# Performance work log

Measured on AMD Instinct MI355X. Metric: run time of the kernel, lower is better.

## Reference

```python
import jax, jax.numpy as jnp
import numpy as np

# model dims (see init_kwargs)
HID = 2048
H = 16
Q_LORA = 768
KV_LORA = 512
QK_NOPE = 128
QK_ROPE = 64
QK_HEAD = QK_NOPE + QK_ROPE  # 192
V_DIM = 128
HI = 8        # indexer heads
DI = 128      # indexer head dim
TOPK = 512    # index_topk
EPS = 1e-5
B, S = 1, 2048


def rms_norm(x, w):
    return x * jax.lax.rsqrt(jnp.mean(x * x, -1, keepdims=True) + EPS) * w


def layer_norm(x, w, b):
    m = jnp.mean(x, -1, keepdims=True)
    v = jnp.mean((x - m) ** 2, -1, keepdims=True)
    return (x - m) * jax.lax.rsqrt(v + EPS) * w + b


def rotate_half(x):
    x1, x2 = jnp.split(x, 2, axis=-1)
    return jnp.concatenate([-x2, x1], axis=-1)


def rope_bshd(x, cos, sin):
    # x: [B,S,H,D], cos/sin: [B,S,D] -> broadcast over heads (unsqueeze_dim=2)
    return x * cos[:, :, None, :] + rotate_half(x) * sin[:, :, None, :]


def setup_inputs() -> dict:
    key = jax.random.key(0)
    ks = jax.random.split(key, 16)
    std = 0.02
    hidden_states = jax.random.normal(ks[0], (B, S, HID), jnp.float32)
    # real RoPE tables, theta=10000, head_dim=QK_ROPE
    inv_freq = 1.0 / (10000.0 ** (np.arange(0, QK_ROPE, 2, dtype=np.float32) / QK_ROPE))
    freqs = np.arange(S, dtype=np.float32)[:, None] * inv_freq[None, :]  # [S, ROPE/2]
    emb = np.concatenate([freqs, freqs], axis=-1)
    cos = jnp.asarray(np.cos(emb))[None]  # [1,S,ROPE]
    sin = jnp.asarray(np.sin(emb))[None]
    w = lambda k, shp: jax.random.normal(k, shp, jnp.float32) * std
    return {
        'hidden_states': hidden_states, 'cos': cos, 'sin': sin,
        'wq_a': w(ks[1], (Q_LORA, HID)),
        'q_a_norm_w': jnp.ones((Q_LORA,), jnp.float32),
        'wq_b': w(ks[2], (H * QK_HEAD, Q_LORA)),
        'wkv_a': w(ks[3], (KV_LORA + QK_ROPE, HID)),
        'kv_a_norm_w': jnp.ones((KV_LORA,), jnp.float32),
        'wkv_b': w(ks[4], (H * (QK_NOPE + V_DIM), KV_LORA)),
        'wo': w(ks[5], (HID, H * V_DIM)),
        'idx_wq_b': w(ks[6], (HI * DI, Q_LORA)),
        'idx_wk': w(ks[7], (DI, HID)),
        'idx_k_norm_w': jnp.ones((DI,), jnp.float32),
        'idx_k_norm_b': jnp.zeros((DI,), jnp.float32),
        'idx_weights_w': w(ks[8], (HI, HID)),
    }


def reference(hidden_states, cos, sin, wq_a, q_a_norm_w, wq_b, wkv_a, kv_a_norm_w,
              wkv_b, wo, idx_wq_b, idx_wk, idx_k_norm_w, idx_k_norm_b, idx_weights_w):
    b, s, _ = hidden_states.shape
    # ---- MLA projections ----
    q_lora = rms_norm(hidden_states @ wq_a.T, q_a_norm_w)              # [B,S,Q_LORA]
    q = (q_lora @ wq_b.T).reshape(b, s, H, QK_HEAD)
    q_nope, q_rope = jnp.split(q, [QK_NOPE], axis=-1)
    q_rope = rope_bshd(q_rope, cos, sin)

    kv = hidden_states @ wkv_a.T                                        # [B,S,KV_LORA+ROPE]
    kv_lat, k_rope = jnp.split(kv, [KV_LORA], axis=-1)
    k_rope = k_rope * cos + rotate_half(k_rope) * sin                   # shared MQA rope key [B,S,ROPE]
    kv_lat = rms_norm(kv_lat, kv_a_norm_w)
    kvb = (kv_lat @ wkv_b.T).reshape(b, s, H, QK_NOPE + V_DIM)
    k_nope, value = jnp.split(kvb, [QK_NOPE], axis=-1)

    queries = jnp.concatenate([q_nope, q_rope], axis=-1)                # [B,S,H,QK_HEAD]
    keys = jnp.concatenate(
        [k_nope, jnp.broadcast_to(k_rope[:, :, None, :], (b, s, H, QK_ROPE))], axis=-1)

    # ---- lightning indexer (DSA): per-query top-k KV selection ----
    iq = (q_lora @ idx_wq_b.T).reshape(b, s, HI, DI)
    iq_rot, iq_pass = jnp.split(iq, [QK_ROPE], axis=-1)
    iq = jnp.concatenate([rope_bshd(iq_rot, cos, sin), iq_pass], axis=-1)
    ik = layer_norm(hidden_states @ idx_wk.T, idx_k_norm_w, idx_k_norm_b)  # [B,S,DI]
    ik_rot, ik_pass = jnp.split(ik, [QK_ROPE], axis=-1)
    ik = jnp.concatenate([ik_rot * cos + rotate_half(ik_rot) * sin, ik_pass], axis=-1)

    iscores = jnp.einsum('bqhd,bkd->bqhk', iq, ik) * (DI ** -0.5)       # [B,S,HI,S]
    iw = (hidden_states @ idx_weights_w.T) * (HI ** -0.5)               # [B,S,HI]
    iscore = jnp.einsum('bqh,bqhk->bqk', iw, iscores)                   # [B,S,S]

    causal = jnp.tril(jnp.ones((s, s), bool))
    iscore = jnp.where(causal[None], iscore, -1e9)
    _, topk_idx = jax.lax.top_k(iscore, TOPK)                           # [B,S,TOPK]
    allow = jnp.zeros((b, s, s), bool).at[
        jnp.arange(b)[:, None, None], jnp.arange(s)[None, :, None], topk_idx].set(True)
    allow = allow & causal[None]                                        # topk AND causal

    # ---- masked attention ----
    scale = QK_HEAD ** -0.5
    scores = jnp.einsum('bqhd,bkhd->bhqk', queries, keys) * scale       # [B,H,S,S]
    scores = jnp.where(allow[:, None], scores, -jnp.inf)
    probs = jax.nn.softmax(scores, axis=-1)
    out = jnp.einsum('bhqk,bkhd->bqhd', probs, value).reshape(b, s, H * V_DIM)
    return out @ wo.T
```

## Files before the change

kernel.cpp:

```cpp
#include <hip/hip_runtime.h>
#include <hip/hip_bf16.h>
#include <stdint.h>
#include <math.h>

#define S_LEN 2048
#define HIDDEN 2048
#define NHEAD 16
#define QLORA 768
#define KVLORA 512
#define QKNOPE 128
#define QKROPE 64
#define QKHEAD 192
#define VDIM 128
#define HIN 8
#define DIN 128
#define TOPKN 512
#define EPSF 1e-5f
#define DLAT 576
#define SCALE_ATT 0.07216878364870322f

typedef __bf16 bf16x8 __attribute__((ext_vector_type(8)));
typedef float  f32x4  __attribute__((ext_vector_type(4)));

static __device__ __forceinline__ float wave_reduce_sum(float v) {
    #pragma unroll
    for (int off = 32; off > 0; off >>= 1) v += __shfl_down(v, off);
    return v;
}

static __device__ __forceinline__ void splitw(__bf16* __restrict__ H,
                                              __bf16* __restrict__ L,
                                              size_t idx, float v) {
    __bf16 h = (__bf16)v;
    H[idx] = h;
    L[idx] = (__bf16)(v - (float)h);
}

#define PREP_BLOCKS 17280
__global__ __launch_bounds__(256) void prep_all(
        const float* __restrict__ hid,     __bf16* hidH,  __bf16* hidL,
        const float* __restrict__ wq_a,    __bf16* wqaH,  __bf16* wqaL,
        const float* __restrict__ idx_wq_b,__bf16* iwqH,  __bf16* iwqL,
        const float* __restrict__ idx_wk,  __bf16* iwkH,  __bf16* iwkL,
        const float* __restrict__ wq_b,    __bf16* wq_b_bf,
        const float* __restrict__ wkv_a,   __bf16* wkv_a_bf,
        const float* __restrict__ wkv_b,   __bf16* wkv_b_bf,
        const float* __restrict__ wo,      __bf16* wo_bf,
        __bf16* wknt) {
    int b = blockIdx.x, tid = threadIdx.x;
    const float* src; __bf16 *dH = nullptr, *dL = nullptr, *dC = nullptr;
    int base;
    if (b < 4096)        { src = hid;      dH = hidH; dL = hidL; base = b; }
    else if (b < 5632)   { src = wq_a;     dH = wqaH; dL = wqaL; base = b - 4096; }
    else if (b < 6400)   { src = idx_wq_b; dH = iwqH; dL = iwqL; base = b - 5632; }
    else if (b < 6656)   { src = idx_wk;   dH = iwkH; dL = iwkL; base = b - 6400; }
    else if (b < 8960)   { src = wq_b;     dC = wq_b_bf;  base = b - 6656; }
    else if (b < 10112)  { src = wkv_a;    dC = wkv_a_bf; base = b - 8960; }
    else if (b < 12160)  { src = wkv_b;    dC = wkv_b_bf; base = b - 10112; }
    else if (b < 16256)  { src = wo;       dC = wo_bf;    base = b - 12160; }
    else {
        int e = ((b - 16256) * 256 + tid) * 4;
        int c = e & 511, d = (e >> 9) & 127, h = e >> 16;
        f32x4 v = *(const f32x4*)(wkv_b + ((size_t)(h * 256 + d)) * 512 + c);
        #pragma unroll
        for (int j = 0; j < 4; ++j)
            wknt[(size_t)h * 65536 + (c + j) * 128 + d] = (__bf16)v[j];
        return;
    }
    int i = (base * 256 + tid) * 4;
    f32x4 v = *(const f32x4*)(src + i);
    if (dC) {
        #pragma unroll
        for (int j = 0; j < 4; ++j) dC[i + j] = (__bf16)v[j];
    } else {
        #pragma unroll
        for (int j = 0; j < 4; ++j) splitw(dH, dL, i + j, v[j]);
    }
}

#define GBM 128
#define GBN 64
#define GBK 32
template <typename OutT>
static __device__ __forceinline__ void gemm_s_core(
        const __bf16* __restrict__ A, const __bf16* __restrict__ B,
        OutT* __restrict__ C, int K, int lda, int ldb, int ldc,
        int bx, int by) {
    __shared__ __bf16 sAs[GBM * GBK];
    __shared__ __bf16 sBs[GBN * GBK];
    int tid = threadIdx.x;
    int lane = tid & 63, wid = tid >> 6;
    int quad = lane >> 4, l16 = lane & 15;
    int wm = wid >> 1, wn = wid & 1;
    int row0 = by * GBM, col0 = bx * GBN;

    f32x4 acc[4][2] = {};
    int am = tid >> 1, ah = tid & 1;
    int bn = tid >> 2, bq = tid & 3;

    for (int k0 = 0; k0 < K; k0 += GBK) {
        const uint4* ga = (const uint4*)(A + (size_t)(row0 + am) * lda + k0 + ah * 16);
        uint4* da = (uint4*)&sAs[am * GBK + ah * 16];
        da[0] = ga[0];
        da[1] = ga[1];
        *(uint4*)&sBs[bn * GBK + bq * 8] =
            *(const uint4*)(B + (size_t)(col0 + bn) * ldb + k0 + bq * 8);
        __syncthreads();
        bf16x8 af[4], bfr[2];
        #pragma unroll
        for (int mi = 0; mi < 4; ++mi)
            af[mi] = *(const bf16x8*)&sAs[(wm * 64 + mi * 16 + l16) * GBK + quad * 8];
        #pragma unroll
        for (int ni = 0; ni < 2; ++ni)
            bfr[ni] = *(const bf16x8*)&sBs[(wn * 32 + ni * 16 + l16) * GBK + quad * 8];
        #pragma unroll
        for (int mi = 0; mi < 4; ++mi)
            #pragma unroll
            for (int ni = 0; ni < 2; ++ni)
                acc[mi][ni] = __builtin_amdgcn_mfma_f32_16x16x32_bf16(
                    af[mi], bfr[ni], acc[mi][ni], 0, 0, 0);
        __syncthreads();
    }
    #pragma unroll
    for (int mi = 0; mi < 4; ++mi)
        #pragma unroll
        for (int ni = 0; ni < 2; ++ni)
            #pragma unroll
            for (int r = 0; r < 4; ++r) {
                int row = row0 + wm * 64 + mi * 16 + quad * 4 + r;
                int col = col0 + wn * 32 + ni * 16 + l16;
                C[(size_t)row * ldc + col] = (OutT)acc[mi][ni][r];
            }
}

template <typename OutT>
__global__ __launch_bounds__(256) void gemm_s(const __bf16* __restrict__ A,
                                              const __bf16* __restrict__ B,
                                              OutT* __restrict__ C,
                                              int K, int lda, int ldb, int ldc,
                                              long sA, long sB, long sC) {
    gemm_s_core<OutT>(A + (size_t)blockIdx.z * sA, B + (size_t)blockIdx.z * sB,
                      C + (size_t)blockIdx.z * sC, K, lda, ldb, ldc,
                      blockIdx.x, blockIdx.y);
}

template <bool CAUSAL>
static __device__ __forceinline__ void gemm3_core(
        const __bf16* __restrict__ Ah, const __bf16* __restrict__ Al,
        const __bf16* __restrict__ Bh, const __bf16* __restrict__ Bl,
        float* __restrict__ C, int K, int lda, int ldb, int ldc,
        int row_base, int bx, int by) {
    int row0 = by * GBM + row_base, col0 = bx * GBN;
    if (CAUSAL && col0 > row0 + GBM - 1) return;
    __shared__ __bf16 sAh[GBM * GBK], sAl[GBM * GBK];
    __shared__ __bf16 sBh[GBN * GBK], sBl[GBN * GBK];
    int tid = threadIdx.x;
    int lane = tid & 63, wid = tid >> 6;
    int quad = lane >> 4, l16 = lane & 15;
    int wm = wid >> 1, wn = wid & 1;

    f32x4 acc[4][2] = {};
    int am = tid >> 1, ah = tid & 1;
    int bn = tid >> 2, bq = tid & 3;

    for (int k0 = 0; k0 < K; k0 += GBK) {
        size_t aoff = (size_t)(row0 + am) * lda + k0 + ah * 16;
        uint4* dah = (uint4*)&sAh[am * GBK + ah * 16];
        uint4* dal = (uint4*)&sAl[am * GBK + ah * 16];
        dah[0] = ((const uint4*)(Ah + aoff))[0];
        dah[1] = ((const uint4*)(Ah + aoff))[1];
        dal[0] = ((const uint4*)(Al + aoff))[0];
        dal[1] = ((const uint4*)(Al + aoff))[1];
        size_t boff = (size_t)(col0 + bn) * ldb + k0 + bq * 8;
        *(uint4*)&sBh[bn * GBK + bq * 8] = *(const uint4*)(Bh + boff);
        *(uint4*)&sBl[bn * GBK + bq * 8] = *(const uint4*)(Bl + boff);
        __syncthreads();
        bf16x8 afh[4], afl[4], bfh[2], bfl[2];
        #pragma unroll
        for (int mi = 0; mi < 4; ++mi) {
            int o = (wm * 64 + mi * 16 + l16) * GBK + quad * 8;
            afh[mi] = *(const bf16x8*)&sAh[o];
            afl[mi] = *(const bf16x8*)&sAl[o];
        }
        #pragma unroll
        for (int ni = 0; ni < 2; ++ni) {
            int o = (wn * 32 + ni * 16 + l16) * GBK + quad * 8;
            bfh[ni] = *(const bf16x8*)&sBh[o];
            bfl[ni] = *(const bf16x8*)&sBl[o];
        }
        #pragma unroll
        for (int mi = 0; mi < 4; ++mi)
            #pragma unroll
            for (int ni = 0; ni < 2; ++ni) {
                acc[mi][ni] = __builtin_amdgcn_mfma_f32_16x16x32_bf16(
                    afl[mi], bfh[ni], acc[mi][ni], 0, 0, 0);
                acc[mi][ni] = __builtin_amdgcn_mfma_f32_16x16x32_bf16(
                    afh[mi], bfl[ni], acc[mi][ni], 0, 0, 0);
                acc[mi][ni] = __builtin_amdgcn_mfma_f32_16x16x32_bf16(
                    afh[mi], bfh[ni], acc[mi][ni], 0, 0, 0);
            }
        __syncthreads();
    }
    #pragma unroll
    for (int mi = 0; mi < 4; ++mi)
        #pragma unroll
        for (int ni = 0; ni < 2; ++ni)
            #pragma unroll
            for (int r = 0; r < 4; ++r) {
                int row = row0 + wm * 64 + mi * 16 + quad * 4 + r;
                int col = col0 + wn * 32 + ni * 16 + l16;
                C[(size_t)row * ldc + col] = acc[mi][ni][r];
            }
}

__global__ __launch_bounds__(256) void gemm3_ks(const __bf16* __restrict__ Ah,
                                                const __bf16* __restrict__ Al,
                                                const __bf16* __restrict__ Bh,
                                                const __bf16* __restrict__ Bl,
                                                float* __restrict__ Cpart,
                                                int Ksub, int lda, int ldb, int ldc,
                                                long sC) {
    int bz = blockIdx.z, koff = bz * Ksub;
    gemm3_core<false>(Ah + koff, Al + koff, Bh + koff, Bl + koff,
                      Cpart + (size_t)bz * sC, Ksub, lda, ldb, ldc, 0,
                      blockIdx.x, blockIdx.y);
}

__global__ __launch_bounds__(256) void fused_mid(
        const __bf16* __restrict__ qlH, const __bf16* __restrict__ qlL,
        const __bf16* __restrict__ wq_b_bf, __bf16* __restrict__ qbuf_bf,
        const __bf16* __restrict__ hidH, const __bf16* __restrict__ hidL,
        const __bf16* __restrict__ wkv_a_bf, float* __restrict__ kv,
        const __bf16* __restrict__ iwqH, const __bf16* __restrict__ iwqL,
        float* __restrict__ iqraw,
        const __bf16* __restrict__ iwkH, const __bf16* __restrict__ iwkL,
        float* __restrict__ ikraw) {
    int b = blockIdx.x;
    if (b < 768) {
        gemm_s_core<__bf16>(qlH, wq_b_bf, qbuf_bf, QLORA, QLORA, QLORA,
                            NHEAD * QKHEAD, b % 48, b / 48);
    } else if (b < 912) {
        int r = b - 768;
        gemm_s_core<float>(hidH, wkv_a_bf, kv, HIDDEN, HIDDEN, HIDDEN, DLAT,
                           r % 9, r / 9);
    } else if (b < 1168) {
        int r = b - 912;
        gemm3_core<false>(qlH, qlL, iwqH, iwqL, iqraw, QLORA, QLORA, QLORA,
                          HIN * DIN, 0, r & 15, r >> 4);
    } else {
        int r = b - 1168;
        gemm3_core<false>(hidH, hidL, iwkH, iwkL, ikraw, HIDDEN, HIDDEN, HIDDEN,
                          DIN, 0, r & 1, r >> 1);
    }
}

__global__ __launch_bounds__(256) void fused2(
        const __bf16* __restrict__ qbuf_bf, const __bf16* __restrict__ wknt,
        __bf16* __restrict__ qeff,
        const __bf16* __restrict__ cqH, const __bf16* __restrict__ cqL,
        const __bf16* __restrict__ ikH, const __bf16* __restrict__ ikL,
        float* __restrict__ iscore) {
    int b = blockIdx.x;
    if (b < 2048) {
        int bx = b & 7, by = (b >> 3) & 15, bz = b >> 7;
        gemm_s_core<__bf16>(qbuf_bf + bz * QKHEAD, wknt + (size_t)bz * 512 * 128,
                            qeff + bz * DLAT, 128, NHEAD * QKHEAD, 128,
                            NHEAD * DLAT, bx, by);
    } else {
        int r = b - 2048;
        gemm3_core<true>(cqH, cqL, ikH, ikL, iscore, DIN, DIN, DIN, S_LEN,
                         TOPKN, r & 31, r >> 5);
    }
}

__global__ __launch_bounds__(256) void rmsnorm_split4(const float* __restrict__ p,
                                                      long ps,
                                                      const float* __restrict__ w,
                                                      __bf16* __restrict__ yH,
                                                      __bf16* __restrict__ yL, int ncols) {
    int row = blockIdx.x, tid = threadIdx.x;
    const float* p0 = p + (size_t)row * ncols;
    float ss = 0.f;
    for (int c = tid; c < ncols; c += 256) {
        float v = p0[c] + p0[ps + c] + p0[2 * ps + c] + p0[3 * ps + c];
        ss += v * v;
    }
    __shared__ float red[4];
    ss = wave_reduce_sum(ss);
    if ((tid & 63) == 0) red[tid >> 6] = ss;
    __syncthreads();
    float tot = red[0] + red[1] + red[2] + red[3];
    float inv = rsqrtf(tot / (float)ncols + EPSF);
    for (int c = tid; c < ncols; c += 256) {
        float v = p0[c] + p0[ps + c] + p0[2 * ps + c] + p0[3 * ps + c];
        splitw(yH, yL, (size_t)row * ncols + c, v * inv * w[c]);
    }
}

__global__ __launch_bounds__(256) void fused_post(
        const __bf16* __restrict__ qbuf, __bf16* __restrict__ qeff,
        const float* __restrict__ kv, const float* __restrict__ kvw,
        __bf16* __restrict__ klat,
        const float* __restrict__ ikraw, const float* __restrict__ lnw,
        const float* __restrict__ lnb, __bf16* __restrict__ ikH, __bf16* __restrict__ ikL,
        const float* __restrict__ iqraw, const float* __restrict__ hid,
        const float* __restrict__ iww, __bf16* __restrict__ cqH, __bf16* __restrict__ cqL,
        const float* __restrict__ cosT, const float* __restrict__ sinT) {
    int s = blockIdx.x, tid = threadIdx.x;
    int lane = tid & 63, wid = tid >> 6;

    for (int i = tid; i < NHEAD * 32; i += 256) {
        int h = i >> 5, d = i & 31;
        const __bf16* base = qbuf + (size_t)s * (NHEAD * QKHEAD) + h * QKHEAD + QKNOPE;
        float x1 = (float)base[d], x2 = (float)base[d + 32];
        float c1 = cosT[s * 64 + d],      s1 = sinT[s * 64 + d];
        float c2 = cosT[s * 64 + d + 32], s2 = sinT[s * 64 + d + 32];
        __bf16* o = qeff + (size_t)s * (NHEAD * DLAT) + h * DLAT + 512;
        o[d]      = (__bf16)(x1 * c1 - x2 * s1);
        o[d + 32] = (__bf16)(x2 * c2 + x1 * s2);
    }

    {
        const float* row = kv + (size_t)s * DLAT;
        float ss = 0.f;
        for (int c = tid; c < KVLORA; c += 256) { float v = row[c]; ss += v * v; }
        __shared__ float redB[4];
        ss = wave_reduce_sum(ss);
        if (lane == 0) redB[wid] = ss;
        __syncthreads();
        float tot = redB[0] + redB[1] + redB[2] + redB[3];
        float inv = rsqrtf(tot / (float)KVLORA + EPSF);
        __bf16* orow = klat + (size_t)s * DLAT;
        for (int c = tid; c < KVLORA; c += 256)
            orow[c] = (__bf16)(row[c] * inv * kvw[c]);
        if (tid < 32) {
            int d = tid;
            float x1 = row[KVLORA + d], x2 = row[KVLORA + d + 32];
            float c1 = cosT[s * 64 + d],      s1 = sinT[s * 64 + d];
            float c2 = cosT[s * 64 + d + 32], s2 = sinT[s * 64 + d + 32];
            orow[512 + d]      = (__bf16)(x1 * c1 - x2 * s1);
            orow[512 + d + 32] = (__bf16)(x2 * c2 + x1 * s2);
        }
    }

    {
        float x = (tid < DIN) ? ikraw[(size_t)s * DIN + tid] : 0.f;
        __shared__ float redC1[4], redC2[4], sy[DIN];
        float sm = wave_reduce_sum(x);
        if (lane == 0) redC1[wid] = sm;
        __syncthreads();
        float mean = (redC1[0] + redC1[1] + redC1[2] + redC1[3]) / (float)DIN;
        float dx = (tid < DIN) ? (x - mean) : 0.f;
        float vs = wave_reduce_sum(dx * dx);
        if (lane == 0) redC2[wid] = vs;
        __syncthreads();
        float var = (redC2[0] + redC2[1] + redC2[2] + redC2[3]) / (float)DIN;
        if (tid < DIN) sy[tid] = dx * rsqrtf(var + EPSF) * lnw[tid] + lnb[tid];
        __syncthreads();
        size_t ro = (size_t)s * DIN;
        if (tid < 32) {
            int d = tid;
            float c1 = cosT[s * 64 + d],      s1 = sinT[s * 64 + d];
            float c2 = cosT[s * 64 + d + 32], s2 = sinT[s * 64 + d + 32];
            splitw(ikH, ikL, ro + d,      sy[d] * c1 - sy[d + 32] * s1);
            splitw(ikH, ikL, ro + d + 32, sy[d + 32] * c2 + sy[d] * s2);
        } else if (tid >= 64 && tid < DIN) {
            splitw(ikH, ikL, ro + tid, sy[tid]);
        }
        __syncthreads();
    }

    {
        __shared__ float redD[4][HIN], siw[HIN];
        float a8[HIN] = {};
        const float* xr = hid + (size_t)s * HIDDEN;
        for (int c = tid; c < HIDDEN; c += 256) {
            float x = xr[c];
            #pragma unroll
            for (int h = 0; h < HIN; ++h) a8[h] += x * iww[h * HIDDEN + c];
        }
        #pragma unroll
        for (int h = 0; h < HIN; ++h) a8[h] = wave_reduce_sum(a8[h]);
        if (lane == 0)
            #pragma unroll
            for (int h = 0; h < HIN; ++h) redD[wid][h] = a8[h];
        __syncthreads();
        if (tid < HIN)
            siw[tid] = redD[0][tid] + redD[1][tid] + redD[2][tid] + redD[3][tid];
        __syncthreads();
        if (tid < DIN) {
            int d = tid;
            float acc = 0.f;
            float c1 = 0.f, s1 = 0.f;
            if (d < 64) { c1 = cosT[s * 64 + d]; s1 = sinT[s * 64 + d]; }
            #pragma unroll
            for (int h = 0; h < HIN; ++h) {
                const float* base = iqraw + ((size_t)s * HIN + h) * DIN;
                float v;
                if (d < 32)       v = base[d] * c1 - base[d + 32] * s1;
                else if (d < 64)  v = base[d] * c1 + base[d - 32] * s1;
                else              v = base[d];
                acc += siw[h] * v;
            }
            splitw(cqH, cqL, (size_t)s * DIN + d, acc * 0.03125f);
        }
    }
}

__global__ __launch_bounds__(256) void topk_rows(const float* __restrict__ iscore,
                                                 int* __restrict__ topk) {
    int q = TOPKN + blockIdx.x;
    int n = q + 1;
    __shared__ uint32_t skey[S_LEN];
    __shared__ int hist[256];
    __shared__ int scan[256];
    __shared__ uint32_t sp;
    __shared__ int sr, pos;
    int tid = threadIdx.x;
    const float* row = iscore + (size_t)q * S_LEN;
    for (int i = tid; i < n; i += 256) {
        uint32_t u = __float_as_uint(row[i]);
        skey[i] = (u & 0x80000000u) ? ~u : (u | 0x80000000u);
    }
    __syncthreads();
    uint32_t prefix = 0;
    int remk = TOPKN;
    for (int pass = 0; pass < 4; ++pass) {
        int shift = 24 - 8 * pass;
        uint32_t pmask = pass ? (0xFFFFFFFFu << (shift + 8)) : 0u;
        hist[tid] = 0;
        __syncthreads();
        for (int i = tid; i < n; i += 256) {
            uint32_t u = skey[i];
            if ((u & pmask) == prefix) atomicAdd(&hist[(u >> shift) & 255], 1);
        }
        __syncthreads();
        scan[tid] = hist[tid];
        __syncthreads();
        for (int step = 1; step < 256; step <<= 1) {
            int v = (tid + step < 256) ? scan[tid + step] : 0;
            __syncthreads();
            scan[tid] += v;
            __syncthreads();
        }
        int Sb = scan[tid];
        int Snext = (tid < 255) ? scan[tid + 1] : 0;
        if (Sb >= remk && Snext < remk) {
            sp = prefix | ((uint32_t)tid << shift);
            sr = remk - Snext;
        }
        __syncthreads();
        prefix = sp; remk = sr;
        __syncthreads();
    }
    if (tid == 0) pos = 0;
    __syncthreads();
    int* orow = topk + (size_t)q * TOPKN;
    for (int i = tid; i < n; i += 256) {
        if (skey[i] > prefix) { int p = atomicAdd(&pos, 1); orow[p] = i; }
    }
    __syncthreads();
    int base = pos;
    int chunk = (n + 255) >> 8;
    int lo = tid * chunk, hiEnd = lo + chunk;
    if (hiEnd > n) hiEnd = n;
    int cnt = 0;
    for (int i = lo; i < hiEnd; ++i) cnt += (skey[i] == prefix);
    scan[tid] = cnt;
    __syncthreads();
    for (int step = 1; step < 256; step <<= 1) {
        int v = (tid >= step) ? scan[tid - step] : 0;
        __syncthreads();
        scan[tid] += v;
        __syncthreads();
    }
    int r = scan[tid] - cnt;
    for (int i = lo; i < hiEnd && r < remk; ++i) {
        if (skey[i] == prefix) { orow[base + r] = i; ++r; }
    }
}

#define SKS 584
__global__ __launch_bounds__(256) void attn2(const __bf16* __restrict__ qeff,
                                             const __bf16* __restrict__ klat,
                                             const int* __restrict__ topk,
                                             __bf16* __restrict__ o_lat) {
    int q = (blockIdx.x * 997) & (S_LEN - 1);
    int tid = threadIdx.x;
    int lane = tid & 63, wid = tid >> 6;
    int l16 = lane & 15, quad = lane >> 4;
    int wn = wid & 1, wk = wid >> 1;

    __shared__ short sK[32 * SKS];
    __shared__ float s_part[2][16][37];
    __shared__ float s_S[16][38];
    __shared__ float s_m[16], s_l[16], s_alpha[16], s_inv[16];

    int L = (q < TOPKN) ? (q + 1) : TOPKN;
    int nt = (L + 31) >> 5;
    const int* idxr = topk + (size_t)q * TOPKN;

    bf16x8 qf[9];
    const __bf16* qrow = qeff + (size_t)q * (NHEAD * DLAT) + l16 * DLAT + wk * 288 + quad * 8;
    #pragma unroll
    for (int s = 0; s < 9; ++s) qf[s] = *(const bf16x8*)(qrow + s * 32);

    if (tid < 16) { s_m[tid] = -1e30f; s_l[tid] = 0.f; }

    f32x4 oacc[8];
    #pragma unroll
    for (int i = 0; i < 8; ++i) oacc[i] = (f32x4){0.f, 0.f, 0.f, 0.f};

    int srow = tid >> 3, schk = tid & 7;

    for (int t = 0; t < nt; ++t) {
        int ki = t * 32 + srow;
        int gk = 0;
        if (ki < L) gk = (q < TOPKN) ? ki : idxr[ki];
        const uint4* src = (const uint4*)(klat + (size_t)gk * DLAT) + schk * 9;
        uint4* dst = (uint4*)((char*)sK + srow * (SKS * 2) + schk * 144);
        #pragma unroll
        for (int c = 0; c < 9; ++c) dst[c] = src[c];
        __syncthreads();

        f32x4 sacc = {0.f, 0.f, 0.f, 0.f};
        const short* kbase = sK + (wn * 16 + l16) * SKS + wk * 288 + quad * 8;
        #pragma unroll
        for (int s = 0; s < 9; ++s) {
            bf16x8 kf = *(const bf16x8*)(kbase + s * 32);
            sacc = __builtin_amdgcn_mfma_f32_16x16x32_bf16(qf[s], kf, sacc, 0, 0, 0);
        }
        #pragma unroll
        for (int r = 0; r < 4; ++r)
            s_part[wk][quad * 4 + r][wn * 16 + l16] = sacc[r];
        __syncthreads();

        {
            int h = tid >> 4, k0 = (tid & 15) * 2;
            float v0 = -1e30f, v1 = -1e30f;
            if (t * 32 + k0 < L)
                v0 = (s_part[0][h][k0] + s_part[1][h][k0]) * SCALE_ATT;
            if (t * 32 + k0 + 1 < L)
                v1 = (s_part[0][h][k0 + 1] + s_part[1][h][k0 + 1]) * SCALE_ATT;
            float mt = fmaxf(v0, v1);
            #pragma unroll
            for (int o = 1; o < 16; o <<= 1) mt = fmaxf(mt, __shfl_xor(mt, o));
            float mold = s_m[h];
            float mnew = fmaxf(mold, mt);
            float p0 = __expf(v0 - mnew), p1 = __expf(v1 - mnew);
            float ls = p0 + p1;
            #pragma unroll
            for (int o = 1; o < 16; o <<= 1) ls += __shfl_xor(ls, o);
            *(float2*)&s_S[h][k0] = make_float2(p0, p1);
            if ((tid & 15) == 0) {
                float alpha = __expf(mold - mnew);
                s_alpha[h] = alpha;
                s_m[h] = mnew;
                s_l[h] = s_l[h] * alpha + ls;
            }
        }
        __syncthreads();

        f32x4 al4 = *(const f32x4*)&s_alpha[quad * 4];
        bf16x8 pf;
        int qhi = quad & 2, qlo = quad & 1;
        #pragma unroll
        for (int p = 0; p < 4; ++p) {
            float2 v = *(const float2*)&s_S[l16][quad * 8 + ((2 * p) ^ qhi)];
            float e0 = qlo ? v.y : v.x, e1 = qlo ? v.x : v.y;
            pf[2 * p]     = (__bf16)e0;
            pf[2 * p + 1] = (__bf16)e1;
        }
        const __bf16* sKb = (const __bf16*)sK;
        #pragma unroll
        for (int n = 0; n < 8; ++n) {
            int dim = wid * 128 + n * 16 + l16;
            bf16x8 vf;
            #pragma unroll
            for (int j = 0; j < 8; ++j)
                vf[j] = sKb[(quad * 8 + (j ^ quad)) * SKS + dim];
            #pragma unroll
            for (int r = 0; r < 4; ++r) oacc[n][r] *= al4[r];
            oacc[n] = __builtin_amdgcn_mfma_f32_16x16x32_bf16(pf, vf, oacc[n], 0, 0, 0);
        }
        __syncthreads();
    }

    if (tid < 16) s_inv[tid] = 1.f / s_l[tid];
    __syncthreads();
    f32x4 inv4 = *(const f32x4*)&s_inv[quad * 4];
    #pragma unroll
    for (int n = 0; n < 8; ++n) {
        int dim = wid * 128 + n * 16 + l16;
        #pragma unroll
        for (int r = 0; r < 4; ++r) {
            int h = quad * 4 + r;
            o_lat[(size_t)q * 8192 + h * 512 + dim] = (__bf16)(oacc[n][r] * inv4[r]);
        }
    }
}

extern "C" void kernel_launch(void* const* d_in, const int* in_sizes, int n_in,
                              void* d_out, int out_size, void* d_ws, size_t ws_size,
                              hipStream_t stream) {
    const float* hid          = (const float*)d_in[0];
    const float* cosT         = (const float*)d_in[1];
    const float* sinT         = (const float*)d_in[2];
    const float* wq_a         = (const float*)d_in[3];
    const float* q_a_norm_w   = (const float*)d_in[4];
    const float* wq_b         = (const float*)d_in[5];
    const float* wkv_a        = (const float*)d_in[6];
    const float* kv_a_norm_w  = (const float*)d_in[7];
    const float* wkv_b        = (const float*)d_in[8];
    const float* wo           = (const float*)d_in[9];
    const float* idx_wq_b     = (const float*)d_in[10];
    const float* idx_wk       = (const float*)d_in[11];
    const float* idx_k_norm_w = (const float*)d_in[12];
    const float* idx_k_norm_b = (const float*)d_in[13];
    const float* idx_weights_w= (const float*)d_in[14];
    float* out = (float*)d_out;

    char* ws = (char*)d_ws;
    size_t off = 0;
    auto alloc = [&](size_t nbytes) {
        void* p = (void*)(ws + off);
        off += (nbytes + 255) & ~(size_t)255;
        return p;
    };
    __bf16* qbuf_bf  = (__bf16*)alloc((size_t)S_LEN * NHEAD * QKHEAD * 2);
    float*  kv       = (float*) alloc((size_t)S_LEN * DLAT * 4);
    __bf16* klat_bf  = (__bf16*)alloc((size_t)S_LEN * DLAT * 2);
    __bf16* qeff_bf  = (__bf16*)alloc((size_t)S_LEN * NHEAD * DLAT * 2);
    int*    topk     = (int*)   alloc((size_t)S_LEN * TOPKN * 4);
    char* uB = (char*)alloc((size_t)S_LEN * HIDDEN * 2 + (size_t)DLAT * HIDDEN * 2);
    __bf16* hidH      = (__bf16*)uB;
    __bf16* wkv_a_bf  = (__bf16*)(uB + (size_t)S_LEN * HIDDEN * 2);
    __bf16* attn_o_bf = (__bf16*)uB;
    __bf16* hidL      = (__bf16*)alloc((size_t)S_LEN * HIDDEN * 2);
    char* uC = (char*)alloc((size_t)S_LEN * NHEAD * 512 * 2);
    float*  qpart    = (float*)uC;
    __bf16* o_lat_bf = (__bf16*)uC;
    float* iqraw  = (float*)uC;
    float* ikraw  = (float*)(uC + 8388608);
    float* iscore = (float*)(uC + 11599872);
    __bf16* wq_b_bf  = (__bf16*)alloc((size_t)(NHEAD * QKHEAD) * QLORA * 2);
    __bf16* wkv_b_bf = (__bf16*)alloc((size_t)(NHEAD * 256) * KVLORA * 2);
    __bf16* wknt_bf  = (__bf16*)alloc((size_t)NHEAD * 512 * 128 * 2);
    __bf16* wo_bf    = (__bf16*)alloc((size_t)HIDDEN * (NHEAD * VDIM) * 2);
    __bf16* wqaH = (__bf16*)alloc((size_t)QLORA * HIDDEN * 2);
    __bf16* wqaL = (__bf16*)alloc((size_t)QLORA * HIDDEN * 2);
    __bf16* qlH  = (__bf16*)alloc((size_t)S_LEN * QLORA * 2);
    __bf16* qlL  = (__bf16*)alloc((size_t)S_LEN * QLORA * 2);
    __bf16* iwqH = (__bf16*)alloc((size_t)(HIN * DIN) * QLORA * 2);
    __bf16* iwqL = (__bf16*)alloc((size_t)(HIN * DIN) * QLORA * 2);
    __bf16* iwkH = (__bf16*)alloc((size_t)DIN * HIDDEN * 2);
    __bf16* iwkL = (__bf16*)alloc((size_t)DIN * HIDDEN * 2);
    __bf16* ikH  = (__bf16*)alloc((size_t)S_LEN * DIN * 2);
    __bf16* ikL  = (__bf16*)alloc((size_t)S_LEN * DIN * 2);
    __bf16* cqH  = (__bf16*)alloc((size_t)S_LEN * DIN * 2);
    __bf16* cqL  = (__bf16*)alloc((size_t)S_LEN * DIN * 2);
    (void)ws_size; (void)in_sizes; (void)n_in; (void)out_size;

    dim3 blk(256);

    prep_all<<<PREP_BLOCKS, blk, 0, stream>>>(
        hid, hidH, hidL, wq_a, wqaH, wqaL, idx_wq_b, iwqH, iwqL,
        idx_wk, iwkH, iwkL, wq_b, wq_b_bf, wkv_a, wkv_a_bf,
        wkv_b, wkv_b_bf, wo, wo_bf, wknt_bf);

    gemm3_ks<<<dim3(QLORA / GBN, S_LEN / GBM, 4), blk, 0, stream>>>(
        hidH, hidL, wqaH, wqaL, qpart, HIDDEN / 4, HIDDEN, HIDDEN, QLORA,
        (long)S_LEN * QLORA);
    rmsnorm_split4<<<S_LEN, 256, 0, stream>>>(qpart, (long)S_LEN * QLORA,
                                              q_a_norm_w, qlH, qlL, QLORA);

    fused_mid<<<1200, blk, 0, stream>>>(qlH, qlL, wq_b_bf, qbuf_bf,
                                        hidH, hidL, wkv_a_bf, kv,
                                        iwqH, iwqL, iqraw, iwkH, iwkL, ikraw);

    fused_post<<<S_LEN, 256, 0, stream>>>(qbuf_bf, qeff_bf, kv, kv_a_norm_w, klat_bf,
                                          ikraw, idx_k_norm_w, idx_k_norm_b, ikH, ikL,
                                          iqraw, hid, idx_weights_w, cqH, cqL,
                                          cosT, sinT);

    fused2<<<2048 + 384, blk, 0, stream>>>(qbuf_bf, wknt_bf, qeff_bf,
                                           cqH, cqL, ikH, ikL, iscore);

    topk_rows<<<S_LEN - TOPKN, 256, 0, stream>>>(iscore, topk);

    attn2<<<S_LEN, 256, 0, stream>>>(qeff_bf, klat_bf, topk, o_lat_bf);

    gemm_s<__bf16><<<dim3(VDIM / GBN, S_LEN / GBM, NHEAD), blk, 0, stream>>>(
        o_lat_bf, wkv_b_bf + 128 * 512, attn_o_bf, 512,
        NHEAD * 512, 512, NHEAD * VDIM, 512, 256 * 512, VDIM);
    gemm_s<float><<<dim3(HIDDEN / GBN, S_LEN / GBM, 1), blk, 0, stream>>>(
        attn_o_bf, wo_bf, out, NHEAD * VDIM,
        NHEAD * VDIM, NHEAD * VDIM, HIDDEN, 0, 0, 0);
}
```

Measured before the change: 572.6 us.

## Use direct global-to-LDS loads in GEMMs and read K/V from global in attention

The GEMM cores now stage A and B tiles with global_load_lds (16-byte direct-to-LDS transfers) instead of loading into registers and storing to shared memory. In the sparse attention kernel, the shared K tile is dropped. Each tile's gathered row indices are written to a small double-buffered LDS array, and K and V fragments are read straight from global memory (through the cache), which removes the staging copy and one barrier per tile. The tradeoff is that V is now read one scalar bf16 at a time per element from global memory, and without the LDS staging this uncoalesced gather may increase memory traffic.

```diff
diff --git a/kernel.cpp b/kernel.cpp
--- a/kernel.cpp
+++ b/kernel.cpp
@@ -34,6 +34,12 @@
     __bf16 h = (__bf16)v;
     H[idx] = h;
     L[idx] = (__bf16)(v - (float)h);
+}
+
+static __device__ __forceinline__ void gll16(const __bf16* g, __bf16* lds_base) {
+    __builtin_amdgcn_global_load_lds(
+        (const __attribute__((address_space(1))) uint32_t*)g,
+        (__attribute__((address_space(3))) uint32_t*)lds_base, 16, 0, 0);
 }
 
 #define PREP_BLOCKS 17280
@@ -93,18 +99,17 @@
     int quad = lane >> 4, l16 = lane & 15;
     int wm = wid >> 1, wn = wid & 1;
     int row0 = by * GBM, col0 = bx * GBN;
+    int lr = lane >> 2, lk = (lane & 3) * 8;
 
     f32x4 acc[4][2] = {};
-    int am = tid >> 1, ah = tid & 1;
-    int bn = tid >> 2, bq = tid & 3;
 
     for (int k0 = 0; k0 < K; k0 += GBK) {
-        const uint4* ga = (const uint4*)(A + (size_t)(row0 + am) * lda + k0 + ah * 16);
-        uint4* da = (uint4*)&sAs[am * GBK + ah * 16];
-        da[0] = ga[0];
-        da[1] = ga[1];
-        *(uint4*)&sBs[bn * GBK + bq * 8] =
-            *(const uint4*)(B + (size_t)(col0 + bn) * ldb + k0 + bq * 8);
+        #pragma unroll
+        for (int c = 0; c < 2; ++c) {
+            int rb = (wid * 2 + c) * 16;
+            gll16(A + (size_t)(row0 + rb + lr) * lda + k0 + lk, sAs + rb * GBK);
+        }
+        gll16(B + (size_t)(col0 + wid * 16 + lr) * ldb + k0 + lk, sBs + wid * 16 * GBK);
         __syncthreads();
         bf16x8 af[4], bfr[2];
         #pragma unroll
@@ -158,22 +163,23 @@
     int lane = tid & 63, wid = tid >> 6;
     int quad = lane >> 4, l16 = lane & 15;
     int wm = wid >> 1, wn = wid & 1;
+    int lr = lane >> 2, lk = (lane & 3) * 8;
 
     f32x4 acc[4][2] = {};
-    int am = tid >> 1, ah = tid & 1;
-    int bn = tid >> 2, bq = tid & 3;
 
     for (int k0 = 0; k0 < K; k0 += GBK) {
-        size_t aoff = (size_t)(row0 + am) * lda + k0 + ah * 16;
-        uint4* dah = (uint4*)&sAh[am * GBK + ah * 16];
-        uint4* dal = (uint4*)&sAl[am * GBK + ah * 16];
-        dah[0] = ((const uint4*)(Ah + aoff))[0];
-        dah[1] = ((const uint4*)(Ah + aoff))[1];
-        dal[0] = ((const uint4*)(Al + aoff))[0];
-        dal[1] = ((const uint4*)(Al + aoff))[1];
-        size_t boff = (size_t)(col0 + bn) * ldb + k0 + bq * 8;
-        *(uint4*)&sBh[bn * GBK + bq * 8] = *(const uint4*)(Bh + boff);
-        *(uint4*)&sBl[bn * GBK + bq * 8] = *(const uint4*)(Bl + boff);
+        #pragma unroll
+        for (int c = 0; c < 2; ++c) {
+            int rb = (wid * 2 + c) * 16;
+            size_t go = (size_t)(row0 + rb + lr) * lda + k0 + lk;
+            gll16(Ah + go, sAh + rb * GBK);
+            gll16(Al + go, sAl + rb * GBK);
+        }
+        {
+            size_t go = (size_t)(col0 + wid * 16 + lr) * ldb + k0 + lk;
+            gll16(Bh + go, sBh + wid * 16 * GBK);
+            gll16(Bl + go, sBl + wid * 16 * GBK);
+        }
         __syncthreads();
         bf16x8 afh[4], afl[4], bfh[2], bfl[2];
         #pragma unroll
@@ -480,7 +486,6 @@
     }
 }
 
-#define SKS 584
 __global__ __launch_bounds__(256) void attn2(const __bf16* __restrict__ qeff,
                                              const __bf16* __restrict__ klat,
                                              const int* __restrict__ topk,
@@ -491,9 +496,9 @@
     int l16 = lane & 15, quad = lane >> 4;
     int wn = wid & 1, wk = wid >> 1;
 
-    __shared__ short sK[32 * SKS];
+    __shared__ int   s_gk[2][32];
     __shared__ float s_part[2][16][37];
-    __shared__ float s_S[16][38];
+    __shared__ float s_S[16][40];
     __shared__ float s_m[16], s_l[16], s_alpha[16], s_inv[16];
 
     int L = (q < TOPKN) ? (q + 1) : TOPKN;
@@ -511,23 +516,21 @@
     #pragma unroll
     for (int i = 0; i < 8; ++i) oacc[i] = (f32x4){0.f, 0.f, 0.f, 0.f};
 
-    int srow = tid >> 3, schk = tid & 7;
-
     for (int t = 0; t < nt; ++t) {
-        int ki = t * 32 + srow;
-        int gk = 0;
-        if (ki < L) gk = (q < TOPKN) ? ki : idxr[ki];
-        const uint4* src = (const uint4*)(klat + (size_t)gk * DLAT) + schk * 9;
-        uint4* dst = (uint4*)((char*)sK + srow * (SKS * 2) + schk * 144);
-        #pragma unroll
-        for (int c = 0; c < 9; ++c) dst[c] = src[c];
-        __syncthreads();
-
+        if (tid < 32) {
+            int ki = t * 32 + tid;
+            int gk = 0;
+            if (ki < L) gk = (q < TOPKN) ? ki : idxr[ki];
+            s_gk[t & 1][tid] = gk;
+        }
+        __syncthreads();
+
+        int myk = s_gk[t & 1][wn * 16 + l16];
+        const __bf16* krow = klat + (size_t)myk * DLAT + wk * 288 + quad * 8;
         f32x4 sacc = {0.f, 0.f, 0.f, 0.f};
-        const short* kbase = sK + (wn * 16 + l16) * SKS + wk * 288 + quad * 8;
         #pragma unroll
         for (int s = 0; s < 9; ++s) {
-            bf16x8 kf = *(const bf16x8*)(kbase + s * 32);
+            bf16x8 kf = *(const bf16x8*)(krow + s * 32);
             sacc = __builtin_amdgcn_mfma_f32_16x16x32_bf16(qf[s], kf, sacc, 0, 0, 0);
         }
         #pragma unroll
@@ -562,28 +565,28 @@
         __syncthreads();
 
         f32x4 al4 = *(const f32x4*)&s_alpha[quad * 4];
+        f32x4 p0v = *(const f32x4*)&s_S[l16][quad * 8];
+        f32x4 p1v = *(const f32x4*)&s_S[l16][quad * 8 + 4];
         bf16x8 pf;
-        int qhi = quad & 2, qlo = quad & 1;
-        #pragma unroll
-        for (int p = 0; p < 4; ++p) {
-            float2 v = *(const float2*)&s_S[l16][quad * 8 + ((2 * p) ^ qhi)];
-            float e0 = qlo ? v.y : v.x, e1 = qlo ? v.x : v.y;
-            pf[2 * p]     = (__bf16)e0;
-            pf[2 * p + 1] = (__bf16)e1;
-        }
-        const __bf16* sKb = (const __bf16*)sK;
+        #pragma unroll
+        for (int i = 0; i < 4; ++i) {
+            pf[i]     = (__bf16)p0v[i];
+            pf[4 + i] = (__bf16)p1v[i];
+        }
+        const __bf16* vb[8];
+        #pragma unroll
+        for (int j = 0; j < 8; ++j)
+            vb[j] = klat + (size_t)s_gk[t & 1][quad * 8 + j] * DLAT;
         #pragma unroll
         for (int n = 0; n < 8; ++n) {
             int dim = wid * 128 + n * 16 + l16;
             bf16x8 vf;
             #pragma unroll
-            for (int j = 0; j < 8; ++j)
-                vf[j] = sKb[(quad * 8 + (j ^ quad)) * SKS + dim];
+            for (int j = 0; j < 8; ++j) vf[j] = vb[j][dim];
             #pragma unroll
             for (int r = 0; r < 4; ++r) oacc[n][r] *= al4[r];
             oacc[n] = __builtin_amdgcn_mfma_f32_16x16x32_bf16(pf, vf, oacc[n], 0, 0, 0);
         }
-        __syncthreads();
     }
 
     if (tid < 16) s_inv[tid] = 1.f / s_l[tid];
```

Result: slower. 620.7 us (+8.4%).
